# Kernel tuning notes

Measured on AMD Instinct MI355X. Metric: run time of the kernel, lower is better.

The kernel has to match this reference:

```python
import jax, jax.numpy as jnp
import numpy as np

B, T, E = 2, 2048, 1024
H = 16
D = E // H  # head_dim = 64


def setup_inputs() -> dict:
    key = jax.random.key(0)
    ks = jax.random.split(key, 9)
    s = 1.0 / np.sqrt(E)
    inp = {"x": jax.random.normal(ks[0], (B, T, E), dtype=jnp.float32)}
    # Linear params (torch nn.Linear: y = x @ W.T + b)
    inp["Wq"] = jax.random.uniform(ks[1], (E, E), jnp.float32, -s, s)
    inp["bq"] = jax.random.uniform(ks[2], (E,), jnp.float32, -s, s)
    inp["Wk"] = jax.random.uniform(ks[3], (E, E), jnp.float32, -s, s)
    inp["bk"] = jax.random.uniform(ks[4], (E,), jnp.float32, -s, s)
    inp["Wv"] = jax.random.uniform(ks[5], (E, E), jnp.float32, -s, s)
    inp["bv"] = jax.random.uniform(ks[6], (E,), jnp.float32, -s, s)
    inp["Wo"] = jax.random.uniform(ks[7], (E, E), jnp.float32, -s, s)
    inp["bo"] = jax.random.uniform(ks[8], (E,), jnp.float32, -s, s)
    return inp


def reference(x, Wq, bq, Wk, bk, Wv, bv, Wo, bo):
    # QKV projections, reshape to [B, H, T, D]
    def split_heads(y):
        return y.reshape(B, T, H, D).transpose(0, 2, 1, 3)

    Q = split_heads(x @ Wq.T + bq)
    K = split_heads(x @ Wk.T + bk)
    V = split_heads(x @ Wv.T + bv)

    scale = 1.0 / jnp.sqrt(jnp.asarray(D, x.dtype))
    scores = jnp.einsum("bhqd,bhkd->bhqk", Q, K) * scale  # [B,H,T,T]
    attn = jax.nn.softmax(scores, axis=-1)
    out = jnp.einsum("bhqk,bhkd->bhqd", attn, V)  # [B,H,T,D]
    out = out.transpose(0, 2, 1, 3).reshape(B, T, E)
    # dropout is identity in eval mode
    return out @ Wo.T + bo
```

## Files before the change

kernel.cpp:

```cpp
#include <hip/hip_runtime.h>
#include <math.h>

#define BB 2
#define TT 2048
#define EE 1024
#define HH 16
#define DD 64
#define MM (BB*TT)
#define KK EE

typedef short bf16x8 __attribute__((ext_vector_type(8)));
typedef float f32x4  __attribute__((ext_vector_type(4)));
typedef float f32x16 __attribute__((ext_vector_type(16)));
typedef unsigned int u32x4 __attribute__((ext_vector_type(4)));

__device__ __forceinline__ unsigned short f2bf(float f) {
  unsigned int u = __float_as_uint(f);
  u = (u + 0x7FFFu + ((u >> 16) & 1u)) >> 16;
  return (unsigned short)u;
}

__device__ __forceinline__ unsigned int cvtpk(float lo, float hi) {
  unsigned int r;
  asm("v_cvt_pk_bf16_f32 %0, %1, %2" : "=v"(r) : "v"(lo), "v"(hi));
  return r;
}

__device__ __forceinline__ void plswap(unsigned int &a, unsigned int &b) {
  asm("v_permlane32_swap_b32 %0, %1" : "+v"(a), "+v"(b));
}

__device__ __forceinline__ void async16(const void* g, void* l) {
  __builtin_amdgcn_global_load_lds(
      (const __attribute__((address_space(1))) unsigned int*)g,
      (__attribute__((address_space(3))) unsigned int*)l, 16, 0, 0);
}

__global__ __launch_bounds__(256) void to_bf16(
    const float* __restrict__ x,  const float* __restrict__ wq,
    const float* __restrict__ wk, const float* __restrict__ wv,
    const float* __restrict__ wo,
    unsigned short* __restrict__ xh, unsigned short* __restrict__ wcat,
    unsigned short* __restrict__ woh)
{
  int c = blockIdx.x * 256 + threadIdx.x;
  const float* src; unsigned short* dst; int off;
  if (c < 1048576) { src = x; dst = xh; off = c; }
  else {
    int r = c - 1048576;
    int w = r >> 18;
    off = r & 262143;
    if      (w == 0) { src = wq; dst = wcat; }
    else if (w == 1) { src = wk; dst = wcat + (1 << 20); }
    else if (w == 2) { src = wv; dst = wcat + (2 << 20); }
    else             { src = wo; dst = woh; }
  }
  float4 v = ((const float4*)src)[off];
  ushort4 h;
  h.x = f2bf(v.x); h.y = f2bf(v.y); h.z = f2bf(v.z); h.w = f2bf(v.w);
  ((ushort4*)dst)[off] = h;
}

template<int MODE>
__global__ __launch_bounds__(512, 6) void gemm_bf16(
    const unsigned short* __restrict__ A, const unsigned short* __restrict__ B,
    const float* __restrict__ b0p, const float* __restrict__ b1p,
    const float* __restrict__ b2p,
    unsigned short* __restrict__ oq, unsigned short* __restrict__ ok,
    unsigned short* __restrict__ ov, float* __restrict__ ofp, float qscale)
{
  constexpr int NT = (MODE == 0) ? 128 : 64;
  constexpr int JN = NT / 32;
  constexpr int BROWS = NT * 32;
  constexpr int TOT = (MODE == 0) ? 16 : 12;
  __shared__ unsigned short S[12288 + 3 * BROWS];

  const int tid  = threadIdx.x;
  const int lane = tid & 63;
  const int wv   = tid >> 6;
  const int col  = lane & 15;
  const int quad = lane >> 4;
  const int wm = (wv & 3) * 32;
  const int wn = (wv >> 2) * (NT / 2);
  const int m0 = blockIdx.x * 128;
  const int n0 = blockIdx.y * NT;

  const int srow = lane >> 2;
  const int sw16 = (((lane & 3) ^ ((lane >> 2) & 3) ^ (lane >> 4)) << 3);
  const int fswA = ((quad ^ (col & 3) ^ (col >> 2)) << 3);

  auto stage = [&](int kt, int slot) {
#pragma unroll
    for (int s = 0; s < 2; ++s) {
      const int t = wv * 2 + s;
      if (t < TOT) {
        const unsigned short* src; int rb, g0, loff;
        if (t < 8) { src = A; rb = t * 16;       g0 = m0; loff = slot * 4096; }
        else       { src = B; rb = (t - 8) * 16; g0 = n0; loff = 12288 + slot * BROWS; }
        async16(src + (size_t)(g0 + rb + srow) * KK + kt + sw16,
                S + loff + rb * 32);
      }
    }
  };

  f32x4 acc[2][JN];
  const f32x4 z = {0.f, 0.f, 0.f, 0.f};
#pragma unroll
  for (int i = 0; i < 2; ++i)
#pragma unroll
    for (int j = 0; j < JN; ++j) acc[i][j] = z;

  stage(0, 0);

#define GBODY(T, SL, S2, DOSTAGE, VMC) do {                                   \
    if (DOSTAGE) stage(((T) + 1) * 32, S2);                                   \
    asm volatile("s_waitcnt vmcnt(" #VMC ")" ::: "memory");                   \
    __builtin_amdgcn_sched_barrier(0);                                        \
    __builtin_amdgcn_s_barrier();                                             \
    __builtin_amdgcn_sched_barrier(0);                                        \
    const unsigned short* Asb = S + (SL) * 4096;                              \
    const unsigned short* Bsb = S + 12288 + (SL) * BROWS;                     \
    bf16x8 bfr[JN];                                                           \
    _Pragma("unroll")                                                         \
    for (int j = 0; j < JN; ++j)                                              \
      bfr[j] = *(const bf16x8*)(Bsb + (wn + j * 16 + col) * 32 + fswA);       \
    _Pragma("unroll")                                                         \
    for (int i = 0; i < 2; ++i) {                                             \
      bf16x8 af = *(const bf16x8*)(Asb + (wm + i * 16 + col) * 32 + fswA);    \
      _Pragma("unroll")                                                       \
      for (int j = 0; j < JN; ++j)                                            \
        acc[i][j] = __builtin_amdgcn_mfma_f32_16x16x32_bf16(af, bfr[j], acc[i][j], 0, 0, 0); \
    }                                                                         \
  } while (0)

  for (int t = 0; t < 30; t += 3) {
    GBODY(t + 0, 0, 1, 1, 2);
    GBODY(t + 1, 1, 2, 1, 2);
    GBODY(t + 2, 2, 0, 1, 2);
  }
  GBODY(30, 0, 1, 1, 2);
  GBODY(31, 1, 0, 0, 0);
#undef GBODY

  unsigned short* Cs = S;
  if (MODE == 0) {
    __syncthreads();
    const int region = n0 >> 10;
    const float* bias = (region == 0) ? b0p : (region == 1) ? b1p : b2p;
    const float scl = (region == 0) ? qscale : 1.0f;
    const int nlbase = n0 & 1023;
    const int h0 = nlbase >> 6;
    const int b = m0 >> 11, t0 = m0 & (TT - 1);
    if (region < 2) {
#pragma unroll
      for (int i = 0; i < 2; ++i)
#pragma unroll
        for (int j = 0; j < 4; ++j) {
          const int nt = wn + j * 16 + col;
          const float bs = bias[nlbase + nt];
#pragma unroll
          for (int r = 0; r < 4; ++r) {
            const int mt = wm + i * 16 + quad * 4 + r;
            Cs[mt * 136 + nt] = f2bf((acc[i][j][r] + bs) * scl);
          }
        }
      __syncthreads();
      unsigned short* dst = (region == 0) ? oq : ok;
#pragma unroll
      for (int s = 0; s < 4; ++s) {
        const int u = s * 512 + tid;
        const int mt = u >> 4, hs = (u >> 3) & 1, ch = u & 7;
        const size_t g = ((size_t)(b * HH + h0 + hs) * TT + t0 + mt) * DD + ch * 8;
        *(uint4*)(dst + g) = *(const uint4*)(Cs + mt * 136 + hs * 64 + ch * 8);
      }
    } else {
#pragma unroll
      for (int i = 0; i < 2; ++i)
#pragma unroll
        for (int j = 0; j < 4; ++j) {
          const int nt = wn + j * 16 + col;
          const float bs = bias[nlbase + nt];
          ushort4 pk;
          pk.x = f2bf(acc[i][j][0] + bs);
          pk.y = f2bf(acc[i][j][1] + bs);
          pk.z = f2bf(acc[i][j][2] + bs);
          pk.w = f2bf(acc[i][j][3] + bs);
          *(ushort4*)(Cs + nt * 136 + wm + i * 16 + quad * 4) = pk;
        }
      __syncthreads();
#pragma unroll
      for (int s = 0; s < 4; ++s) {
        const int u = s * 512 + tid;
        const int nt = u >> 4, ch = u & 15;
        const int d = nt & 63, hs = nt >> 6;
        const size_t g = ((size_t)(b * HH + h0 + hs) * DD + d) * TT + t0 + ch * 8;
        *(uint4*)(ov + g) = *(const uint4*)(Cs + nt * 136 + ch * 8);
      }
    }
  } else {
#pragma unroll
    for (int i = 0; i < 2; ++i) {
#pragma unroll
      for (int j = 0; j < JN; ++j) {
        const int n = n0 + wn + j * 16 + col;
        const float bs = b0p[n];
#pragma unroll
        for (int r = 0; r < 4; ++r) {
          const int m = m0 + wm + i * 16 + quad * 4 + r;
          ofp[(size_t)m * EE + n] = acc[i][j][r] + bs;
        }
      }
    }
  }
}

__global__ __launch_bounds__(512, 4) void flash_mfma(
    const unsigned short* __restrict__ Qb, const unsigned short* __restrict__ Kb,
    const unsigned short* __restrict__ Vtb, unsigned short* __restrict__ ctx)
{
  __shared__ unsigned short Qs[128 * 64];
  __shared__ unsigned short Ks[4][64 * 64];
  __shared__ unsigned short Vts[4][64 * 64];

  const int tid  = threadIdx.x;
  const int lane = tid & 63;
  const int wv   = tid >> 6;
  const int lq   = lane & 31;
  const int hf   = lane >> 5;
  const int wq   = wv & 3;
  const int wk2  = wv >> 2;
  const int gid  = blockIdx.x;
  const int bh   = gid & 31;
  const int q0   = (gid >> 5) * 128;

  const unsigned short* Qg = Qb  + (size_t)bh * TT * DD;
  const unsigned short* Kg = Kb  + (size_t)bh * TT * DD;
  const unsigned short* Vg = Vtb + (size_t)bh * DD * TT;

  const int srow = lane >> 3;
  const int swb  = ((lane & 7) ^ (lane >> 3)) << 3;

  const int rbK = wq * 16;
  const bool isK = (wv < 4);
  const int sw0 = swb ^ ((((rbK    ) >> 3) & 7) << 3);
  const int sw1 = swb ^ ((((rbK + 8) >> 3) & 7) << 3);
  const unsigned short* g0 =
      (isK ? Kg + (size_t)(rbK + srow) * DD : Vg + (size_t)(rbK + srow) * TT) + sw0;
  const unsigned short* g1 =
      (isK ? Kg + (size_t)(rbK + 8 + srow) * DD : Vg + (size_t)(rbK + 8 + srow) * TT) + sw1;
  unsigned short* l0 = (isK ? &Ks[0][0] : &Vts[0][0]) + rbK * 64;
  unsigned short* l1 = l0 + 8 * 64;
  const int gstep = isK ? 64 * DD : 64;

  auto stage_kv = [&](int ti, int slot) {
    const size_t go = (size_t)ti * gstep;
    async16(g0 + go, l0 + slot * 4096);
    async16(g1 + go, l1 + slot * 4096);
  };

  const int l7 = lane & 7;
  const int d3 = lq >> 3;
  int koff[4], voff[2][2];
#pragma unroll
  for (int s = 0; s < 4; ++s)
    koff[s] = ((wk2 * 32 + lq) * 64 +
               (((2 * s + hf) ^ l7 ^ ((wk2 * 4 + d3) & 7)) << 3)) * 2;
#pragma unroll
  for (int m = 0; m < 2; ++m)
#pragma unroll
    for (int sg = 0; sg < 2; ++sg)
      voff[m][sg] = ((m * 32 + lq) * 64 +
                     (((wk2 * 4 + 2 * sg + hf) ^ l7 ^ ((m * 4 + d3) & 7)) << 3)) * 2;

#pragma unroll
  for (int s = 0; s < 2; ++s) {
    const int rb = wv * 16 + s * 8;
    const int sq = swb ^ (((rb >> 3) & 7) << 3);
    async16(Qg + (size_t)(q0 + rb + srow) * DD + sq, &Qs[rb * 64]);
  }
  stage_kv(0, 0);
  stage_kv(1, 1);
  __syncthreads();

  bf16x8 aq[4];
#pragma unroll
  for (int s = 0; s < 4; ++s)
    aq[s] = *(const bf16x8*)(Qs + (wq * 32 + lq) * 64 +
                             (((2 * s + hf) ^ l7 ^ ((wq * 4 + d3) & 7)) << 3));

  const f32x16 z16 = {0.f,0.f,0.f,0.f,0.f,0.f,0.f,0.f,
                      0.f,0.f,0.f,0.f,0.f,0.f,0.f,0.f};
  f32x16 o_acc[2], sacc, nsacc;
  o_acc[0] = z16; o_acc[1] = z16;
  float lpart = 0.f;

  {
    const char* Kp = (const char*)&Ks[0][0];
    bf16x8 ak = *(const bf16x8*)(Kp + koff[0]);
    sacc = __builtin_amdgcn_mfma_f32_32x32x16_bf16(ak, aq[0], z16, 0, 0, 0);
#pragma unroll
    for (int s = 1; s < 4; ++s) {
      ak = *(const bf16x8*)(Kp + koff[s]);
      sacc = __builtin_amdgcn_mfma_f32_32x32x16_bf16(ak, aq[s], sacc, 0, 0, 0);
    }
  }

#define BODY(T, S0, S1, S2, DOSTAGE, DOQK, VMC, SIN, SOUT) do {               \
    if (DOSTAGE) stage_kv((T) + 2, S2);                                       \
    asm volatile("s_waitcnt vmcnt(" #VMC ")" ::: "memory");                   \
    __builtin_amdgcn_sched_barrier(0);                                        \
    __builtin_amdgcn_s_barrier();                                             \
    __builtin_amdgcn_sched_barrier(0);                                        \
    bf16x8 pa0, pa1;                                                          \
    {      \
      float e0 = __builtin_amdgcn_exp2f(SIN[0]);                              \
      float e1 = __builtin_amdgcn_exp2f(SIN[1]);                              \
      float e2 = __builtin_amdgcn_exp2f(SIN[2]);                              \
      float e3 = __builtin_amdgcn_exp2f(SIN[3]);                              \
      float e4 = __builtin_amdgcn_exp2f(SIN[4]);                              \
      float e5 = __builtin_amdgcn_exp2f(SIN[5]);                              \
      float e6 = __builtin_amdgcn_exp2f(SIN[6]);                              \
      float e7 = __builtin_amdgcn_exp2f(SIN[7]);                              \
      lpart += ((e0 + e1) + (e2 + e3)) + ((e4 + e5) + (e6 + e7));             \
      unsigned int a0 = cvtpk(e0, e1), b0 = cvtpk(e4, e5);                    \
      unsigned int a1 = cvtpk(e2, e3), b1 = cvtpk(e6, e7);                    \
      plswap(a0, b0); plswap(a1, b1);                                         \
      u32x4 w = {a0, a1, b0, b1};                                             \
      pa0 = __builtin_bit_cast(bf16x8, w);                                    \
    }                                                                         \
    {                                                     \
      float e0 = __builtin_amdgcn_exp2f(SIN[8]);                              \
      float e1 = __builtin_amdgcn_exp2f(SIN[9]);                              \
      float e2 = __builtin_amdgcn_exp2f(SIN[10]);                             \
      float e3 = __builtin_amdgcn_exp2f(SIN[11]);                             \
      float e4 = __builtin_amdgcn_exp2f(SIN[12]);                             \
      float e5 = __builtin_amdgcn_exp2f(SIN[13]);                             \
      float e6 = __builtin_amdgcn_exp2f(SIN[14]);                             \
      float e7 = __builtin_amdgcn_exp2f(SIN[15]);                             \
      lpart += ((e0 + e1) + (e2 + e3)) + ((e4 + e5) + (e6 + e7));             \
      unsigned int a0 = cvtpk(e0, e1), b0 = cvtpk(e4, e5);                    \
      unsigned int a1 = cvtpk(e2, e3), b1 = cvtpk(e6, e7);                    \
      plswap(a0, b0); plswap(a1, b1);                                         \
      u32x4 w = {a0, a1, b0, b1};                                             \
      pa1 = __builtin_bit_cast(bf16x8, w);                                    \
    }                                                                         \
    __builtin_amdgcn_s_setprio(1);                                            \
    if (DOQK) {     \
      const char* Kp = (const char*)&Ks[S1][0];                               \
      bf16x8 ak = *(const bf16x8*)(Kp + koff[0]);                             \
      SOUT = __builtin_amdgcn_mfma_f32_32x32x16_bf16(ak, aq[0], z16, 0, 0, 0);\
      _Pragma("unroll")                                                       \
      for (int s = 1; s < 4; ++s) {                                           \
        ak = *(const bf16x8*)(Kp + koff[s]);                                  \
        SOUT = __builtin_amdgcn_mfma_f32_32x32x16_bf16(ak, aq[s], SOUT, 0, 0, 0); \
      }                                                                       \
    }                                                                         \
    {                                                              \
      const char* Vp = (const char*)&Vts[S0][0];                              \
      _Pragma("unroll")                                                       \
      for (int m = 0; m < 2; ++m) {                                           \
        bf16x8 v0 = *(const bf16x8*)(Vp + voff[m][0]);                        \
        bf16x8 v1 = *(const bf16x8*)(Vp + voff[m][1]);                        \
        o_acc[m] = __builtin_amdgcn_mfma_f32_32x32x16_bf16(pa0, v0, o_acc[m], 0, 0, 0); \
        o_acc[m] = __builtin_amdgcn_mfma_f32_32x32x16_bf16(pa1, v1, o_acc[m], 0, 0, 0); \
      }                                                                       \
    }                                                                         \
    __builtin_amdgcn_s_setprio(0);                                            \
  } while (0)

  for (int t = 0; t < 28; t += 4) {
    BODY(t + 0, 0, 1, 2, 1, 1, 2, sacc, nsacc);
    BODY(t + 1, 1, 2, 3, 1, 1, 2, nsacc, sacc);
    BODY(t + 2, 2, 3, 0, 1, 1, 2, sacc, nsacc);
    BODY(t + 3, 3, 0, 1, 1, 1, 2, nsacc, sacc);
  }
  BODY(28, 0, 1, 2, 1, 1, 2, sacc, nsacc);
  BODY(29, 1, 2, 3, 1, 1, 2, nsacc, sacc);
  BODY(30, 2, 3, 0, 0, 1, 0, sacc, nsacc);
  BODY(31, 3, 0, 1, 0, 0, 0, nsacc, sacc);
#undef BODY

  float* Qf = (float*)&Qs[0];
  float* Of = (float*)&Ks[0][0];
  unsigned short* Cs = &Vts[0][0];
  const int bq = bh >> 4, head = bh & 15;

  float lw = lpart + __shfl_xor(lpart, 32);
  if (lane < 32) Qf[wv * 32 + lane] = lw;
  __syncthreads();

  if (wv >= 4) {
#pragma unroll
    for (int m = 0; m < 2; ++m)
#pragma unroll
      for (int r = 0; r < 16; ++r) {
        const int ql = (r & 3) + 8 * (r >> 2) + 4 * hf;
        Of[wq * 2048 + ql * 64 + m * 32 + lq] = o_acc[m][r];
      }
  }
  __syncthreads();

  if (wv < 4) {
    float linv[16];
#pragma unroll
    for (int r = 0; r < 16; ++r) {
      const int ql = (r & 3) + 8 * (r >> 2) + 4 * hf;
      linv[r] = 1.0f / (Qf[wv * 32 + ql] + Qf[(wv + 4) * 32 + ql]);
    }
#pragma unroll
    for (int m = 0; m < 2; ++m)
#pragma unroll
      for (int r = 0; r < 16; ++r) {
        const int ql = (r & 3) + 8 * (r >> 2) + 4 * hf;
        const float val =
            (o_acc[m][r] + Of[wq * 2048 + ql * 64 + m * 32 + lq]) * linv[r];
        const int row = wq * 32 + ql, d = m * 32 + lq;
        Cs[row * 64 + (((d >> 3) ^ (row & 7)) << 3) + (d & 7)] = f2bf(val);
      }
  }
  __syncthreads();

#pragma unroll
  for (int s = 0; s < 2; ++s) {
    const int u = s * 512 + tid;
    const int mr = u >> 3, ch = u & 7;
    const size_t g = ((size_t)(bq * TT + q0 + mr)) * EE + head * DD + ch * 8;
    const int chs = (ch ^ (mr & 7)) << 3;
    *(uint4*)(ctx + g) = *(const uint4*)(Cs + mr * 64 + chs);
  }
}

extern "C" void kernel_launch(void* const* d_in, const int* in_sizes, int n_in,
                              void* d_out, int out_size, void* d_ws, size_t ws_size,
                              hipStream_t stream) {
  const float* x  = (const float*)d_in[0];
  const float* Wq = (const float*)d_in[1];
  const float* bq = (const float*)d_in[2];
  const float* Wk = (const float*)d_in[3];
  const float* bk = (const float*)d_in[4];
  const float* Wv = (const float*)d_in[5];
  const float* bv = (const float*)d_in[6];
  const float* Wo = (const float*)d_in[7];
  const float* bo = (const float*)d_in[8];

  unsigned short* p = (unsigned short*)d_ws;
  const size_t XN = (size_t)MM * EE;
  const size_t WN = (size_t)EE * EE;
  unsigned short* x_h    = p;           p += XN;
  unsigned short* Wcat_h = p;           p += 3 * WN;
  unsigned short* Wo_h   = p;           p += WN;
  unsigned short* Qb     = p;           p += XN;
  unsigned short* Kb     = p;           p += XN;
  unsigned short* Vtb    = p;           p += XN;
  unsigned short* ctx_h  = x_h;

  to_bf16<<<8192, 256, 0, stream>>>(x, Wq, Wk, Wv, Wo, x_h, Wcat_h, Wo_h);

  const float qscale = 0.125f * 1.44269504088896f;

  gemm_bf16<0><<<dim3(MM / 128, 3 * EE / 128), 512, 0, stream>>>(
      x_h, Wcat_h, bq, bk, bv, Qb, Kb, Vtb, nullptr, qscale);

  flash_mfma<<<dim3((TT / 128) * BB * HH), 512, 0, stream>>>(Qb, Kb, Vtb, ctx_h);

  gemm_bf16<2><<<dim3(MM / 128, EE / 64), 512, 0, stream>>>(
      ctx_h, Wo_h, bo, nullptr, nullptr,
      nullptr, nullptr, nullptr, (float*)d_out, 1.0f);
}
```

Baseline: 184.3 us.

## Fuse four kernels into two cooperative persistent kernels with grid sync

Merges the bf16 conversion and the QKV GEMM into one cooperative kernel, and the flash attention and output projection GEMM into another. Grid-wide syncs replace kernel boundaries, and tiles are walked by a persistent grid-stride loop over a grid sized from the occupancy query. The aim is to cut kernel launch gaps and tail effects. The cost is grid-sync overhead, occupancy limited by the larger shared footprint, and the extra loop and sync code in each kernel.

After: 484.2 us. +162.7%, slower.

```diff
diff --git a/kernel.cpp b/kernel.cpp
--- a/kernel.cpp
+++ b/kernel.cpp
@@ -1,5 +1,8 @@
 #include <hip/hip_runtime.h>
+#include <hip/hip_cooperative_groups.h>
 #include <math.h>
+
+namespace cg = cooperative_groups;
 
 #define BB 2
 #define TT 2048
@@ -36,44 +39,18 @@
       (__attribute__((address_space(3))) unsigned int*)l, 16, 0, 0);
 }
 
-__global__ __launch_bounds__(256) void to_bf16(
-    const float* __restrict__ x,  const float* __restrict__ wq,
-    const float* __restrict__ wk, const float* __restrict__ wv,
-    const float* __restrict__ wo,
-    unsigned short* __restrict__ xh, unsigned short* __restrict__ wcat,
-    unsigned short* __restrict__ woh)
-{
-  int c = blockIdx.x * 256 + threadIdx.x;
-  const float* src; unsigned short* dst; int off;
-  if (c < 1048576) { src = x; dst = xh; off = c; }
-  else {
-    int r = c - 1048576;
-    int w = r >> 18;
-    off = r & 262143;
-    if      (w == 0) { src = wq; dst = wcat; }
-    else if (w == 1) { src = wk; dst = wcat + (1 << 20); }
-    else if (w == 2) { src = wv; dst = wcat + (2 << 20); }
-    else             { src = wo; dst = woh; }
-  }
-  float4 v = ((const float4*)src)[off];
-  ushort4 h;
-  h.x = f2bf(v.x); h.y = f2bf(v.y); h.z = f2bf(v.z); h.w = f2bf(v.w);
-  ((ushort4*)dst)[off] = h;
-}
-
 template<int MODE>
-__global__ __launch_bounds__(512, 6) void gemm_bf16(
-    const unsigned short* __restrict__ A, const unsigned short* __restrict__ B,
-    const float* __restrict__ b0p, const float* __restrict__ b1p,
-    const float* __restrict__ b2p,
-    unsigned short* __restrict__ oq, unsigned short* __restrict__ ok,
-    unsigned short* __restrict__ ov, float* __restrict__ ofp, float qscale)
+__device__ __forceinline__ void gemm_body(
+    unsigned short* S, int m0, int n0,
+    const unsigned short* A, const unsigned short* B,
+    const float* b0p, const float* b1p, const float* b2p,
+    unsigned short* oq, unsigned short* ok, unsigned short* ov,
+    float* ofp, float qscale)
 {
   constexpr int NT = (MODE == 0) ? 128 : 64;
   constexpr int JN = NT / 32;
   constexpr int BROWS = NT * 32;
   constexpr int TOT = (MODE == 0) ? 16 : 12;
-  __shared__ unsigned short S[12288 + 3 * BROWS];
 
   const int tid  = threadIdx.x;
   const int lane = tid & 63;
@@ -82,8 +59,6 @@
   const int quad = lane >> 4;
   const int wm = (wv & 3) * 32;
   const int wn = (wv >> 2) * (NT / 2);
-  const int m0 = blockIdx.x * 128;
-  const int n0 = blockIdx.y * NT;
 
   const int srow = lane >> 2;
   const int sw16 = (((lane & 3) ^ ((lane >> 2) & 3) ^ (lane >> 4)) << 3);
@@ -212,15 +187,17 @@
       }
     }
   }
-}
-
-__global__ __launch_bounds__(512, 4) void flash_mfma(
-    const unsigned short* __restrict__ Qb, const unsigned short* __restrict__ Kb,
-    const unsigned short* __restrict__ Vtb, unsigned short* __restrict__ ctx)
+  __syncthreads();
+}
+
+__device__ __forceinline__ void flash_body(
+    int gid, unsigned short* BLOB,
+    const unsigned short* Qb, const unsigned short* Kb,
+    const unsigned short* Vtb, unsigned short* ctx)
 {
-  __shared__ unsigned short Qs[128 * 64];
-  __shared__ unsigned short Ks[4][64 * 64];
-  __shared__ unsigned short Vts[4][64 * 64];
+  unsigned short* Qs   = BLOB;
+  unsigned short* Ksb  = BLOB + 8192;
+  unsigned short* Vtsb = BLOB + 24576;
 
   const int tid  = threadIdx.x;
   const int lane = tid & 63;
@@ -229,7 +206,6 @@
   const int hf   = lane >> 5;
   const int wq   = wv & 3;
   const int wk2  = wv >> 2;
-  const int gid  = blockIdx.x;
   const int bh   = gid & 31;
   const int q0   = (gid >> 5) * 128;
 
@@ -248,7 +224,7 @@
       (isK ? Kg + (size_t)(rbK + srow) * DD : Vg + (size_t)(rbK + srow) * TT) + sw0;
   const unsigned short* g1 =
       (isK ? Kg + (size_t)(rbK + 8 + srow) * DD : Vg + (size_t)(rbK + 8 + srow) * TT) + sw1;
-  unsigned short* l0 = (isK ? &Ks[0][0] : &Vts[0][0]) + rbK * 64;
+  unsigned short* l0 = (isK ? Ksb : Vtsb) + rbK * 64;
   unsigned short* l1 = l0 + 8 * 64;
   const int gstep = isK ? 64 * DD : 64;
 
@@ -295,7 +271,7 @@
   float lpart = 0.f;
 
   {
-    const char* Kp = (const char*)&Ks[0][0];
+    const char* Kp = (const char*)Ksb;
     bf16x8 ak = *(const bf16x8*)(Kp + koff[0]);
     sacc = __builtin_amdgcn_mfma_f32_32x32x16_bf16(ak, aq[0], z16, 0, 0, 0);
 #pragma unroll
@@ -345,8 +321,8 @@
       pa1 = __builtin_bit_cast(bf16x8, w);                                    \
     }                                                                         \
     __builtin_amdgcn_s_setprio(1);                                            \
-    if (DOQK) {     \
-      const char* Kp = (const char*)&Ks[S1][0];                               \
+    if (DOQK) {                                 \
+      const char* Kp = (const char*)(Ksb + (S1) * 4096);                      \
       bf16x8 ak = *(const bf16x8*)(Kp + koff[0]);                             \
       SOUT = __builtin_amdgcn_mfma_f32_32x32x16_bf16(ak, aq[0], z16, 0, 0, 0);\
       _Pragma("unroll")                                                       \
@@ -356,7 +332,7 @@
       }                                                                       \
     }                                                                         \
     {                                                              \
-      const char* Vp = (const char*)&Vts[S0][0];                              \
+      const char* Vp = (const char*)(Vtsb + (S0) * 4096);                     \
       _Pragma("unroll")                                                       \
       for (int m = 0; m < 2; ++m) {                                           \
         bf16x8 v0 = *(const bf16x8*)(Vp + voff[m][0]);                        \
@@ -380,9 +356,9 @@
   BODY(31, 3, 0, 1, 0, 0, 0, nsacc, sacc);
 #undef BODY
 
-  float* Qf = (float*)&Qs[0];
-  float* Of = (float*)&Ks[0][0];
-  unsigned short* Cs = &Vts[0][0];
+  float* Qf = (float*)Qs;
+  float* Of = (float*)Ksb;
+  unsigned short* Cs = Vtsb;
   const int bq = bh >> 4, head = bh & 15;
 
   float lw = lpart + __shfl_xor(lpart, 32);
@@ -427,6 +403,70 @@
     const size_t g = ((size_t)(bq * TT + q0 + mr)) * EE + head * DD + ch * 8;
     const int chs = (ch ^ (mr & 7)) << 3;
     *(uint4*)(ctx + g) = *(const uint4*)(Cs + mr * 64 + chs);
+  }
+  __syncthreads();
+}
+
+__global__ __launch_bounds__(512, 6) void qkv_fused(
+    const float* __restrict__ x,  const float* __restrict__ wq,
+    const float* __restrict__ wk, const float* __restrict__ wv,
+    const float* __restrict__ wo,
+    const float* __restrict__ bqp, const float* __restrict__ bkp,
+    const float* __restrict__ bvp,
+    unsigned short* __restrict__ xh, unsigned short* __restrict__ wcat,
+    unsigned short* __restrict__ woh,
+    unsigned short* __restrict__ oq, unsigned short* __restrict__ ok,
+    unsigned short* __restrict__ ov, float qscale)
+{
+  __shared__ unsigned short S[24576];
+
+  const int gsz = gridDim.x * 512;
+  for (int c = blockIdx.x * 512 + threadIdx.x; c < 2097152; c += gsz) {
+    const float* src; unsigned short* dst; int off;
+    if (c < 1048576) { src = x; dst = xh; off = c; }
+    else {
+      int r = c - 1048576;
+      int w = r >> 18;
+      off = r & 262143;
+      if      (w == 0) { src = wq; dst = wcat; }
+      else if (w == 1) { src = wk; dst = wcat + (1 << 20); }
+      else if (w == 2) { src = wv; dst = wcat + (2 << 20); }
+      else             { src = wo; dst = woh; }
+    }
+    float4 v = ((const float4*)src)[off];
+    ushort4 h;
+    h.x = f2bf(v.x); h.y = f2bf(v.y); h.z = f2bf(v.z); h.w = f2bf(v.w);
+    ((ushort4*)dst)[off] = h;
+  }
+  __threadfence();
+  cg::this_grid().sync();
+
+  for (int tile = blockIdx.x; tile < 768; tile += gridDim.x) {
+    const int m0 = (tile & 31) * 128;
+    const int n0 = (tile >> 5) * 128;
+    gemm_body<0>(S, m0, n0, xh, wcat, bqp, bkp, bvp, oq, ok, ov, nullptr, qscale);
+  }
+}
+
+__global__ __launch_bounds__(512, 4) void attn_out_fused(
+    const unsigned short* __restrict__ Qb, const unsigned short* __restrict__ Kb,
+    const unsigned short* __restrict__ Vtb, unsigned short* __restrict__ ctx,
+    const unsigned short* __restrict__ woh, const float* __restrict__ bop,
+    float* __restrict__ outp)
+{
+  __shared__ unsigned short BLOB[40960];
+
+  for (int g = blockIdx.x; g < 512; g += gridDim.x)
+    flash_body(g, BLOB, Qb, Kb, Vtb, ctx);
+
+  __threadfence();
+  cg::this_grid().sync();
+
+  for (int g = blockIdx.x; g < 512; g += gridDim.x) {
+    const int m0 = (g & 31) * 128;
+    const int n0 = (g >> 5) * 64;
+    gemm_body<2>(BLOB, m0, n0, ctx, woh, bop, nullptr, nullptr,
+                 nullptr, nullptr, nullptr, outp, 1.0f);
   }
 }
 
@@ -442,6 +482,7 @@
   const float* bv = (const float*)d_in[6];
   const float* Wo = (const float*)d_in[7];
   const float* bo = (const float*)d_in[8];
+  float* outp = (float*)d_out;
 
   unsigned short* p = (unsigned short*)d_ws;
   const size_t XN = (size_t)MM * EE;
@@ -454,16 +495,28 @@
   unsigned short* Vtb    = p;           p += XN;
   unsigned short* ctx_h  = x_h;
 
-  to_bf16<<<8192, 256, 0, stream>>>(x, Wq, Wk, Wv, Wo, x_h, Wcat_h, Wo_h);
-
-  const float qscale = 0.125f * 1.44269504088896f;
-
-  gemm_bf16<0><<<dim3(MM / 128, 3 * EE / 128), 512, 0, stream>>>(
-      x_h, Wcat_h, bq, bk, bv, Qb, Kb, Vtb, nullptr, qscale);
-
-  flash_mfma<<<dim3((TT / 128) * BB * HH), 512, 0, stream>>>(Qb, Kb, Vtb, ctx_h);
-
-  gemm_bf16<2><<<dim3(MM / 128, EE / 64), 512, 0, stream>>>(
-      ctx_h, Wo_h, bo, nullptr, nullptr,
-      nullptr, nullptr, nullptr, (float*)d_out, 1.0f);
-}
+  float qscale = 0.125f * 1.44269504088896f;
+
+  int nb1 = 0, nb2 = 0;
+  (void)hipOccupancyMaxActiveBlocksPerMultiprocessor(
+      &nb1, reinterpret_cast<const void*>(&qkv_fused), 512, 0);
+  (void)hipOccupancyMaxActiveBlocksPerMultiprocessor(
+      &nb2, reinterpret_cast<const void*>(&attn_out_fused), 512, 0);
+  int g1 = nb1 * 256; if (g1 > 768 || g1 <= 0) g1 = (g1 <= 0) ? 256 : 768;
+  int g2 = nb2 * 256; if (g2 > 512 || g2 <= 0) g2 = (g2 <= 0) ? 256 : 512;
+
+  {
+    void* args[] = {(void*)&x, (void*)&Wq, (void*)&Wk, (void*)&Wv, (void*)&Wo,
+                    (void*)&bq, (void*)&bk, (void*)&bv,
+                    (void*)&x_h, (void*)&Wcat_h, (void*)&Wo_h,
+                    (void*)&Qb, (void*)&Kb, (void*)&Vtb, (void*)&qscale};
+    hipLaunchCooperativeKernel(reinterpret_cast<const void*>(&qkv_fused),
+                               dim3(g1), dim3(512), args, 0, stream);
+  }
+  {
+    void* args[] = {(void*)&Qb, (void*)&Kb, (void*)&Vtb, (void*)&ctx_h,
+                    (void*)&Wo_h, (void*)&bo, (void*)&outp};
+    hipLaunchCooperativeKernel(reinterpret_cast<const void*>(&attn_out_fused),
+                               dim3(g2), dim3(512), args, 0, stream);
+  }
+}
```

## Fuse fp32-to-bf16 conversion into QKV GEMM loads and drop separate cast kernel

Applied to the files above, without the earlier changes.

Removes the standalone to_bf16 pass. The new qkv_gemm loads fp32 x and weight tiles straight from global memory, converts them to bf16 in registers with v_cvt_pk_bf16_f32, and stores them to LDS with register-level prefetch of the next K-tile, replacing the async global_load_lds path. The Wo conversion is done as a grid-strided tail in the same kernel. This cuts one launch and a full write-then-read of bf16 copies of x and the weights. In exchange the GEMM moves twice the global bytes per tile, gives up async LDS loads, and does the conversion redundantly across blocks that share tiles.

Result: slower. 216.0 us (+17.2%).

```diff
diff --git a/kernel.cpp b/kernel.cpp
--- a/kernel.cpp
+++ b/kernel.cpp
@@ -36,29 +36,162 @@
       (__attribute__((address_space(3))) unsigned int*)l, 16, 0, 0);
 }
 
-__global__ __launch_bounds__(256) void to_bf16(
-    const float* __restrict__ x,  const float* __restrict__ wq,
-    const float* __restrict__ wk, const float* __restrict__ wv,
-    const float* __restrict__ wo,
-    unsigned short* __restrict__ xh, unsigned short* __restrict__ wcat,
-    unsigned short* __restrict__ woh)
+__global__ __launch_bounds__(512, 6) void qkv_gemm(
+    const float* __restrict__ xf,
+    const float* __restrict__ wqf, const float* __restrict__ wkf,
+    const float* __restrict__ wvf, const float* __restrict__ wof,
+    const float* __restrict__ b0p, const float* __restrict__ b1p,
+    const float* __restrict__ b2p,
+    unsigned short* __restrict__ oq, unsigned short* __restrict__ ok,
+    unsigned short* __restrict__ ov, unsigned short* __restrict__ woh,
+    float qscale)
 {
-  int c = blockIdx.x * 256 + threadIdx.x;
-  const float* src; unsigned short* dst; int off;
-  if (c < 1048576) { src = x; dst = xh; off = c; }
-  else {
-    int r = c - 1048576;
-    int w = r >> 18;
-    off = r & 262143;
-    if      (w == 0) { src = wq; dst = wcat; }
-    else if (w == 1) { src = wk; dst = wcat + (1 << 20); }
-    else if (w == 2) { src = wv; dst = wcat + (2 << 20); }
-    else             { src = wo; dst = woh; }
-  }
-  float4 v = ((const float4*)src)[off];
-  ushort4 h;
-  h.x = f2bf(v.x); h.y = f2bf(v.y); h.z = f2bf(v.z); h.w = f2bf(v.w);
-  ((ushort4*)dst)[off] = h;
+  __shared__ unsigned short S[17408];
+
+  const int tid  = threadIdx.x;
+  const int lane = tid & 63;
+  const int wv   = tid >> 6;
+  const int col  = lane & 15;
+  const int quad = lane >> 4;
+  const int wm = (wv & 3) * 32;
+  const int wn = (wv >> 2) * 64;
+  const int m0 = blockIdx.x * 128;
+  const int n0 = blockIdx.y * 128;
+  const int region = n0 >> 10;
+  const int nlocal = n0 & 1023;
+
+  const float* wsrc = (region == 0) ? wqf : (region == 1) ? wkf : wvf;
+
+  const int srow = lane >> 2;
+  const int sw16 = (((lane & 3) ^ ((lane >> 2) & 3) ^ (lane >> 4)) << 3);
+  const int fswA = ((quad ^ (col & 3) ^ (col >> 2)) << 3);
+
+  const bool isA = (wv < 4);
+  const int rb0 = (isA ? (wv * 2) : (wv * 2 - 8)) * 16;
+  const float* gsrc = isA ? xf : wsrc;
+  const float* gp0 = gsrc + (size_t)((isA ? m0 : nlocal) + rb0 + srow) * KK + sw16;
+  const float* gp1 = gp0 + (size_t)16 * KK;
+  unsigned short* lp0 = S + (isA ? 0 : 8192) + rb0 * 32 + lane * 8;
+  unsigned short* lp1 = lp0 + 16 * 32;
+
+  float4 la0 = *(const float4*)(gp0);
+  float4 lb0 = *(const float4*)(gp0 + 4);
+  float4 la1 = *(const float4*)(gp1);
+  float4 lb1 = *(const float4*)(gp1 + 4);
+
+  f32x4 acc[2][4];
+  const f32x4 z = {0.f, 0.f, 0.f, 0.f};
+#pragma unroll
+  for (int i = 0; i < 2; ++i)
+#pragma unroll
+    for (int j = 0; j < 4; ++j) acc[i][j] = z;
+
+#define QBODY(T, SL, DOISSUE) do {                                            \
+    {                         \
+      u32x4 w0, w1;                                                           \
+      w0[0] = cvtpk(la0.x, la0.y); w0[1] = cvtpk(la0.z, la0.w);               \
+      w0[2] = cvtpk(lb0.x, lb0.y); w0[3] = cvtpk(lb0.z, lb0.w);               \
+      w1[0] = cvtpk(la1.x, la1.y); w1[1] = cvtpk(la1.z, la1.w);               \
+      w1[2] = cvtpk(lb1.x, lb1.y); w1[3] = cvtpk(lb1.z, lb1.w);               \
+      *(u32x4*)(lp0 + (SL) * 4096) = w0;                                      \
+      *(u32x4*)(lp1 + (SL) * 4096) = w1;                                      \
+    }                                                                         \
+    if (DOISSUE) {    \
+      const int kt = ((T) + 1) * 32;                                          \
+      la0 = *(const float4*)(gp0 + kt);                                       \
+      lb0 = *(const float4*)(gp0 + kt + 4);                                   \
+      la1 = *(const float4*)(gp1 + kt);                                       \
+      lb1 = *(const float4*)(gp1 + kt + 4);                                   \
+    }                                                                         \
+    asm volatile("s_waitcnt lgkmcnt(0)" ::: "memory");                        \
+    __builtin_amdgcn_sched_barrier(0);                                        \
+    __builtin_amdgcn_s_barrier();                                             \
+    __builtin_amdgcn_sched_barrier(0);                                        \
+    const unsigned short* Asb = S + (SL) * 4096;                              \
+    const unsigned short* Bsb = S + 8192 + (SL) * 4096;                       \
+    bf16x8 bfr[4];                                                            \
+    _Pragma("unroll")                                                         \
+    for (int j = 0; j < 4; ++j)                                               \
+      bfr[j] = *(const bf16x8*)(Bsb + (wn + j * 16 + col) * 32 + fswA);       \
+    _Pragma("unroll")                                                         \
+    for (int i = 0; i < 2; ++i) {                                             \
+      bf16x8 af = *(const bf16x8*)(Asb + (wm + i * 16 + col) * 32 + fswA);    \
+      _Pragma("unroll")                                                       \
+      for (int j = 0; j < 4; ++j)                                             \
+        acc[i][j] = __builtin_amdgcn_mfma_f32_16x16x32_bf16(af, bfr[j], acc[i][j], 0, 0, 0); \
+    }                                                                         \
+    __syncthreads();              \
+  } while (0)
+
+  for (int t = 0; t < 30; t += 2) {
+    QBODY(t + 0, 0, 1);
+    QBODY(t + 1, 1, 1);
+  }
+  QBODY(30, 0, 1);
+  QBODY(31, 1, 0);
+#undef QBODY
+
+  unsigned short* Cs = S;
+  {
+    const float* bias = (region == 0) ? b0p : (region == 1) ? b1p : b2p;
+    const float scl = (region == 0) ? qscale : 1.0f;
+    const int h0 = nlocal >> 6;
+    const int b = m0 >> 11, t0 = m0 & (TT - 1);
+    if (region < 2) {
+#pragma unroll
+      for (int i = 0; i < 2; ++i)
+#pragma unroll
+        for (int j = 0; j < 4; ++j) {
+          const int nt = wn + j * 16 + col;
+          const float bs = bias[nlocal + nt];
+#pragma unroll
+          for (int r = 0; r < 4; ++r) {
+            const int mt = wm + i * 16 + quad * 4 + r;
+            Cs[mt * 136 + nt] = f2bf((acc[i][j][r] + bs) * scl);
+          }
+        }
+      __syncthreads();
+      unsigned short* dst = (region == 0) ? oq : ok;
+#pragma unroll
+      for (int s = 0; s < 4; ++s) {
+        const int u = s * 512 + tid;
+        const int mt = u >> 4, hs = (u >> 3) & 1, ch = u & 7;
+        const size_t g = ((size_t)(b * HH + h0 + hs) * TT + t0 + mt) * DD + ch * 8;
+        *(uint4*)(dst + g) = *(const uint4*)(Cs + mt * 136 + hs * 64 + ch * 8);
+      }
+    } else {
+#pragma unroll
+      for (int i = 0; i < 2; ++i)
+#pragma unroll
+        for (int j = 0; j < 4; ++j) {
+          const int nt = wn + j * 16 + col;
+          const float bs = bias[nlocal + nt];
+          ushort4 pk;
+          pk.x = f2bf(acc[i][j][0] + bs);
+          pk.y = f2bf(acc[i][j][1] + bs);
+          pk.z = f2bf(acc[i][j][2] + bs);
+          pk.w = f2bf(acc[i][j][3] + bs);
+          *(ushort4*)(Cs + nt * 136 + wm + i * 16 + quad * 4) = pk;
+        }
+      __syncthreads();
+#pragma unroll
+      for (int s = 0; s < 4; ++s) {
+        const int u = s * 512 + tid;
+        const int nt = u >> 4, ch = u & 15;
+        const int d = nt & 63, hs = nt >> 6;
+        const size_t g = ((size_t)(b * HH + h0 + hs) * DD + d) * TT + t0 + ch * 8;
+        *(uint4*)(ov + g) = *(const uint4*)(Cs + nt * 136 + ch * 8);
+      }
+    }
+  }
+
+  const int bid = blockIdx.y * gridDim.x + blockIdx.x;
+  for (int c = bid * 512 + tid; c < 262144; c += 768 * 512) {
+    float4 v = ((const float4*)wof)[c];
+    ushort4 h;
+    h.x = f2bf(v.x); h.y = f2bf(v.y); h.z = f2bf(v.z); h.w = f2bf(v.w);
+    ((ushort4*)woh)[c] = h;
+  }
 }
 
 template<int MODE>
@@ -345,7 +478,7 @@
       pa1 = __builtin_bit_cast(bf16x8, w);                                    \
     }                                                                         \
     __builtin_amdgcn_s_setprio(1);                                            \
-    if (DOQK) {     \
+    if (DOQK) {                                 \
       const char* Kp = (const char*)&Ks[S1][0];                               \
       bf16x8 ak = *(const bf16x8*)(Kp + koff[0]);                             \
       SOUT = __builtin_amdgcn_mfma_f32_32x32x16_bf16(ak, aq[0], z16, 0, 0, 0);\
@@ -454,12 +587,10 @@
   unsigned short* Vtb    = p;           p += XN;
   unsigned short* ctx_h  = x_h;
 
-  to_bf16<<<8192, 256, 0, stream>>>(x, Wq, Wk, Wv, Wo, x_h, Wcat_h, Wo_h);
-
   const float qscale = 0.125f * 1.44269504088896f;
 
-  gemm_bf16<0><<<dim3(MM / 128, 3 * EE / 128), 512, 0, stream>>>(
-      x_h, Wcat_h, bq, bk, bv, Qb, Kb, Vtb, nullptr, qscale);
+  qkv_gemm<<<dim3(MM / 128, 3 * EE / 128), 512, 0, stream>>>(
+      x, Wq, Wk, Wv, Wo, bq, bk, bv, Qb, Kb, Vtb, Wo_h, qscale);
 
   flash_mfma<<<dim3((TT / 128) * BB * HH), 512, 0, stream>>>(Qb, Kb, Vtb, ctx_h);
 
```

## Process two KV tiles per barrier in flash attention and add dedicated output GEMM

Applied to the files above, without the earlier changes.

The flash attention loop now handles two K/V tiles per barrier region. It computes both QK^T products first, then softmax and PV for each, and stages the next two tiles at once. This replaces the earlier software-pipelined one-tile-per-barrier scheme with its cross-iteration score carry. The output projection moves to a new specialised gemm_out kernel with 4-slot staging, two k-steps per barrier and 6-block occupancy bounds. Halving the barriers reduces sync overhead, but it also removes the QK/PV overlap across iterations and waits on vmcnt(0).

Result: slower. 188.7 us (+2.4%).

```diff
diff --git a/kernel.cpp b/kernel.cpp
--- a/kernel.cpp
+++ b/kernel.cpp
@@ -214,6 +214,97 @@
   }
 }
 
+__global__ __launch_bounds__(512, 6) void gemm_out(
+    const unsigned short* __restrict__ A, const unsigned short* __restrict__ B,
+    const float* __restrict__ bias, float* __restrict__ ofp)
+{
+  __shared__ unsigned short S[24576];
+
+  const int tid  = threadIdx.x;
+  const int lane = tid & 63;
+  const int wv   = tid >> 6;
+  const int col  = lane & 15;
+  const int quad = lane >> 4;
+  const int wm = (wv & 3) * 32;
+  const int wn = (wv >> 2) * 32;
+  const int m0 = blockIdx.x * 128;
+  const int n0 = blockIdx.y * 64;
+
+  const int srow = lane >> 2;
+  const int sw16 = (((lane & 3) ^ ((lane >> 2) & 3) ^ (lane >> 4)) << 3);
+  const int fswA = ((quad ^ (col & 3) ^ (col >> 2)) << 3);
+
+  auto stage = [&](int kt, int slot) {
+#pragma unroll
+    for (int s = 0; s < 2; ++s) {
+      const int t = wv * 2 + s;
+      if (t < 12) {
+        const unsigned short* src; int rb, g0, loff;
+        if (t < 8) { src = A; rb = t * 16;       g0 = m0; loff = slot * 4096; }
+        else       { src = B; rb = (t - 8) * 16; g0 = n0; loff = 16384 + slot * 2048; }
+        async16(src + (size_t)(g0 + rb + srow) * KK + kt + sw16,
+                S + loff + rb * 32);
+      }
+    }
+  };
+
+  f32x4 acc[2][2];
+  const f32x4 z = {0.f, 0.f, 0.f, 0.f};
+#pragma unroll
+  for (int i = 0; i < 2; ++i)
+#pragma unroll
+    for (int j = 0; j < 2; ++j) acc[i][j] = z;
+
+  stage(0, 0);
+  stage(32, 1);
+
+#define GCOMP(SL) do {                                                        \
+    const unsigned short* Asb = S + (SL) * 4096;                              \
+    const unsigned short* Bsb = S + 16384 + (SL) * 2048;                      \
+    bf16x8 b0 = *(const bf16x8*)(Bsb + (wn + col) * 32 + fswA);               \
+    bf16x8 b1 = *(const bf16x8*)(Bsb + (wn + 16 + col) * 32 + fswA);          \
+    _Pragma("unroll")                                                         \
+    for (int i = 0; i < 2; ++i) {                                             \
+      bf16x8 af = *(const bf16x8*)(Asb + (wm + i * 16 + col) * 32 + fswA);    \
+      acc[i][0] = __builtin_amdgcn_mfma_f32_16x16x32_bf16(af, b0, acc[i][0], 0, 0, 0); \
+      acc[i][1] = __builtin_amdgcn_mfma_f32_16x16x32_bf16(af, b1, acc[i][1], 0, 0, 0); \
+    }                                                                         \
+} while (0)
+
+#define REGION2(T, SLa, SLb, SSa, SSb, DOSTAGE, VMC) do {                     \
+    asm volatile("s_waitcnt vmcnt(" #VMC ")" ::: "memory");                   \
+    __builtin_amdgcn_sched_barrier(0);                                        \
+    __builtin_amdgcn_s_barrier();                                             \
+    __builtin_amdgcn_sched_barrier(0);                                        \
+    if (DOSTAGE) { stage(((T) + 2) * 32, SSa); stage(((T) + 3) * 32, SSb); }  \
+    GCOMP(SLa);                                                               \
+    GCOMP(SLb);                                                               \
+} while (0)
+
+  for (int t = 0; t < 28; t += 4) {
+    REGION2(t + 0, 0, 1, 2, 3, 1, 0);
+    REGION2(t + 2, 2, 3, 0, 1, 1, 0);
+  }
+  REGION2(28, 0, 1, 2, 3, 1, 0);
+  REGION2(30, 2, 3, 0, 1, 0, 0);
+#undef REGION2
+#undef GCOMP
+
+#pragma unroll
+  for (int i = 0; i < 2; ++i) {
+#pragma unroll
+    for (int j = 0; j < 2; ++j) {
+      const int n = n0 + wn + j * 16 + col;
+      const float bs = bias[n];
+#pragma unroll
+      for (int r = 0; r < 4; ++r) {
+        const int m = m0 + wm + i * 16 + quad * 4 + r;
+        ofp[(size_t)m * EE + n] = acc[i][j][r] + bs;
+      }
+    }
+  }
+}
+
 __global__ __launch_bounds__(512, 4) void flash_mfma(
     const unsigned short* __restrict__ Qb, const unsigned short* __restrict__ Kb,
     const unsigned short* __restrict__ Vtb, unsigned short* __restrict__ ctx)
@@ -290,29 +381,12 @@
 
   const f32x16 z16 = {0.f,0.f,0.f,0.f,0.f,0.f,0.f,0.f,
                       0.f,0.f,0.f,0.f,0.f,0.f,0.f,0.f};
-  f32x16 o_acc[2], sacc, nsacc;
+  f32x16 o_acc[2];
   o_acc[0] = z16; o_acc[1] = z16;
   float lpart = 0.f;
 
-  {
-    const char* Kp = (const char*)&Ks[0][0];
-    bf16x8 ak = *(const bf16x8*)(Kp + koff[0]);
-    sacc = __builtin_amdgcn_mfma_f32_32x32x16_bf16(ak, aq[0], z16, 0, 0, 0);
-#pragma unroll
-    for (int s = 1; s < 4; ++s) {
-      ak = *(const bf16x8*)(Kp + koff[s]);
-      sacc = __builtin_amdgcn_mfma_f32_32x32x16_bf16(ak, aq[s], sacc, 0, 0, 0);
-    }
-  }
-
-#define BODY(T, S0, S1, S2, DOSTAGE, DOQK, VMC, SIN, SOUT) do {               \
-    if (DOSTAGE) stage_kv((T) + 2, S2);                                       \
-    asm volatile("s_waitcnt vmcnt(" #VMC ")" ::: "memory");                   \
-    __builtin_amdgcn_sched_barrier(0);                                        \
-    __builtin_amdgcn_s_barrier();                                             \
-    __builtin_amdgcn_sched_barrier(0);                                        \
-    bf16x8 pa0, pa1;                                                          \
-    {      \
+#define SMPACK(SIN, PA0, PA1) do {                                            \
+    {                                                                         \
       float e0 = __builtin_amdgcn_exp2f(SIN[0]);                              \
       float e1 = __builtin_amdgcn_exp2f(SIN[1]);                              \
       float e2 = __builtin_amdgcn_exp2f(SIN[2]);                              \
@@ -326,9 +400,9 @@
       unsigned int a1 = cvtpk(e2, e3), b1 = cvtpk(e6, e7);                    \
       plswap(a0, b0); plswap(a1, b1);                                         \
       u32x4 w = {a0, a1, b0, b1};                                             \
-      pa0 = __builtin_bit_cast(bf16x8, w);                                    \
+      PA0 = __builtin_bit_cast(bf16x8, w);                                    \
     }                                                                         \
-    {                                                     \
+    {                                                                         \
       float e0 = __builtin_amdgcn_exp2f(SIN[8]);                              \
       float e1 = __builtin_amdgcn_exp2f(SIN[9]);                              \
       float e2 = __builtin_amdgcn_exp2f(SIN[10]);                             \
@@ -342,43 +416,64 @@
       unsigned int a1 = cvtpk(e2, e3), b1 = cvtpk(e6, e7);                    \
       plswap(a0, b0); plswap(a1, b1);                                         \
       u32x4 w = {a0, a1, b0, b1};                                             \
-      pa1 = __builtin_bit_cast(bf16x8, w);                                    \
+      PA1 = __builtin_bit_cast(bf16x8, w);                                    \
     }                                                                         \
+} while (0)
+
+#define QKT(SL, SOUT) do {                                                    \
+    const char* Kp = (const char*)&Ks[SL][0];                                 \
+    bf16x8 ak = *(const bf16x8*)(Kp + koff[0]);                               \
+    SOUT = __builtin_amdgcn_mfma_f32_32x32x16_bf16(ak, aq[0], z16, 0, 0, 0);  \
+    _Pragma("unroll")                                                         \
+    for (int s = 1; s < 4; ++s) {                                             \
+      ak = *(const bf16x8*)(Kp + koff[s]);                                    \
+      SOUT = __builtin_amdgcn_mfma_f32_32x32x16_bf16(ak, aq[s], SOUT, 0, 0, 0); \
+    }                                                                         \
+} while (0)
+
+#define PVT(SL, P0, P1) do {                                                  \
+    const char* Vp = (const char*)&Vts[SL][0];                                \
+    _Pragma("unroll")                                                         \
+    for (int m = 0; m < 2; ++m) {                                             \
+      bf16x8 v0 = *(const bf16x8*)(Vp + voff[m][0]);                          \
+      bf16x8 v1 = *(const bf16x8*)(Vp + voff[m][1]);                          \
+      o_acc[m] = __builtin_amdgcn_mfma_f32_32x32x16_bf16(P0, v0, o_acc[m], 0, 0, 0); \
+      o_acc[m] = __builtin_amdgcn_mfma_f32_32x32x16_bf16(P1, v1, o_acc[m], 0, 0, 0); \
+    }                                                                         \
+} while (0)
+
+#define REGION(T, SLa, SLb, SSa, SSb, DOSTAGE) do {                           \
+    asm volatile("s_waitcnt vmcnt(0)" ::: "memory");                          \
+    __builtin_amdgcn_sched_barrier(0);                                        \
+    __builtin_amdgcn_s_barrier();                                             \
+    __builtin_amdgcn_sched_barrier(0);                                        \
+    if (DOSTAGE) { stage_kv((T) + 2, SSa); stage_kv((T) + 3, SSb); }          \
+    f32x16 sa, sb;                                                            \
     __builtin_amdgcn_s_setprio(1);                                            \
-    if (DOQK) {     \
-      const char* Kp = (const char*)&Ks[S1][0];                               \
-      bf16x8 ak = *(const bf16x8*)(Kp + koff[0]);                             \
-      SOUT = __builtin_amdgcn_mfma_f32_32x32x16_bf16(ak, aq[0], z16, 0, 0, 0);\
-      _Pragma("unroll")                                                       \
-      for (int s = 1; s < 4; ++s) {                                           \
-        ak = *(const bf16x8*)(Kp + koff[s]);                                  \
-        SOUT = __builtin_amdgcn_mfma_f32_32x32x16_bf16(ak, aq[s], SOUT, 0, 0, 0); \
-      }                                                                       \
-    }                                                                         \
-    {                                                              \
-      const char* Vp = (const char*)&Vts[S0][0];                              \
-      _Pragma("unroll")                                                       \
-      for (int m = 0; m < 2; ++m) {                                           \
-        bf16x8 v0 = *(const bf16x8*)(Vp + voff[m][0]);                        \
-        bf16x8 v1 = *(const bf16x8*)(Vp + voff[m][1]);                        \
-        o_acc[m] = __builtin_amdgcn_mfma_f32_32x32x16_bf16(pa0, v0, o_acc[m], 0, 0, 0); \
-        o_acc[m] = __builtin_amdgcn_mfma_f32_32x32x16_bf16(pa1, v1, o_acc[m], 0, 0, 0); \
-      }                                                                       \
-    }                                                                         \
+    QKT(SLa, sa);                                                             \
+    QKT(SLb, sb);                                                             \
     __builtin_amdgcn_s_setprio(0);                                            \
-  } while (0)
+    bf16x8 pa0, pa1, pb0, pb1;                                                \
+    SMPACK(sa, pa0, pa1);                                                     \
+    __builtin_amdgcn_s_setprio(1);                                            \
+    PVT(SLa, pa0, pa1);                                                       \
+    __builtin_amdgcn_s_setprio(0);                                            \
+    SMPACK(sb, pb0, pb1);                                                     \
+    __builtin_amdgcn_s_setprio(1);                                            \
+    PVT(SLb, pb0, pb1);                                                       \
+    __builtin_amdgcn_s_setprio(0);                                            \
+} while (0)
 
   for (int t = 0; t < 28; t += 4) {
-    BODY(t + 0, 0, 1, 2, 1, 1, 2, sacc, nsacc);
-    BODY(t + 1, 1, 2, 3, 1, 1, 2, nsacc, sacc);
-    BODY(t + 2, 2, 3, 0, 1, 1, 2, sacc, nsacc);
-    BODY(t + 3, 3, 0, 1, 1, 1, 2, nsacc, sacc);
-  }
-  BODY(28, 0, 1, 2, 1, 1, 2, sacc, nsacc);
-  BODY(29, 1, 2, 3, 1, 1, 2, nsacc, sacc);
-  BODY(30, 2, 3, 0, 0, 1, 0, sacc, nsacc);
-  BODY(31, 3, 0, 1, 0, 0, 0, nsacc, sacc);
-#undef BODY
+    REGION(t + 0, 0, 1, 2, 3, 1);
+    REGION(t + 2, 2, 3, 0, 1, 1);
+  }
+  REGION(28, 0, 1, 2, 3, 1);
+  REGION(30, 2, 3, 0, 1, 0);
+#undef REGION
+#undef PVT
+#undef QKT
+#undef SMPACK
 
   float* Qf = (float*)&Qs[0];
   float* Of = (float*)&Ks[0][0];
@@ -454,16 +549,15 @@
   unsigned short* Vtb    = p;           p += XN;
   unsigned short* ctx_h  = x_h;
 
+  const float qscale = 0.125f * 1.44269504088896f;
+
   to_bf16<<<8192, 256, 0, stream>>>(x, Wq, Wk, Wv, Wo, x_h, Wcat_h, Wo_h);
-
-  const float qscale = 0.125f * 1.44269504088896f;
 
   gemm_bf16<0><<<dim3(MM / 128, 3 * EE / 128), 512, 0, stream>>>(
       x_h, Wcat_h, bq, bk, bv, Qb, Kb, Vtb, nullptr, qscale);
 
   flash_mfma<<<dim3((TT / 128) * BB * HH), 512, 0, stream>>>(Qb, Kb, Vtb, ctx_h);
 
-  gemm_bf16<2><<<dim3(MM / 128, EE / 64), 512, 0, stream>>>(
-      ctx_h, Wo_h, bo, nullptr, nullptr,
-      nullptr, nullptr, nullptr, (float*)d_out, 1.0f);
-}
+  gemm_out<<<dim3(MM / 128, EE / 64), 512, 0, stream>>>(
+      ctx_h, Wo_h, bo, (float*)d_out);
+}
```
